# Kernel optimization log

Hardware: AMD Instinct MI355X
Metric: run time of the kernel (lower is better)

## Reference

```python
import jax, jax.numpy as jnp
import numpy as np

D_MODEL = 64
N_HEAD = 4
HEAD_DIM = D_MODEL // N_HEAD  # 16


def setup_inputs() -> dict:
    key = jax.random.key(0)
    ks = jax.random.split(key, 8)
    B, T_dec, T_enc = 16, 1024, 1024
    s = 1.0 / np.sqrt(D_MODEL)
    return {
        "x": jax.random.normal(ks[0], (B, T_dec, D_MODEL), dtype=jnp.float32),
        "encoder_outputs": jax.random.normal(ks[1], (B, T_enc, D_MODEL), dtype=jnp.float32),
        "encoder_outputs_mask": jnp.ones((B, T_enc), dtype=jnp.int32),
        "Wkv": jax.random.normal(ks[2], (D_MODEL, 2 * D_MODEL), dtype=jnp.float32) * s,
        "bkv": jnp.zeros((2 * D_MODEL,), dtype=jnp.float32),
        "Wq": jax.random.normal(ks[3], (D_MODEL, D_MODEL), dtype=jnp.float32) * s,
        "bq": jnp.zeros((D_MODEL,), dtype=jnp.float32),
        "Wproj": jax.random.normal(ks[4], (D_MODEL, D_MODEL), dtype=jnp.float32) * s,
        "bproj": jnp.zeros((D_MODEL,), dtype=jnp.float32),
    }


def reference(x, encoder_outputs, encoder_outputs_mask, Wkv, bkv, Wq, bq, Wproj, bproj):
    B, T_dec, C = x.shape
    T_enc = encoder_outputs.shape[1]
    kv = encoder_outputs @ Wkv + bkv                      # [B, T_enc, 2C]
    k, v = kv[..., :D_MODEL], kv[..., D_MODEL:]          # [B, T_enc, C]
    q = x @ Wq + bq                                      # [B, T_dec, C]
    q = q.reshape(B, T_dec, N_HEAD, HEAD_DIM)
    k = k.reshape(B, T_enc, N_HEAD, HEAD_DIM)
    v = v.reshape(B, T_enc, N_HEAD, HEAD_DIM)
    scale = 1.0 / jnp.sqrt(jnp.asarray(HEAD_DIM, dtype=q.dtype))
    att = jnp.einsum("bqhd,bkhd->bhqk", q, k) * scale    # [B, H, T_dec, T_enc]
    mask = (encoder_outputs_mask == 0)[:, None, None, :]  # [B, 1, 1, T_enc]
    att = jnp.where(mask, jnp.asarray(-jnp.inf, dtype=att.dtype), att)
    att = jax.nn.softmax(att, axis=-1)
    ctx = jnp.einsum("bhqk,bkhd->bqhd", att, v).reshape(B, T_dec, C)
    # dropout is identity at eval time
    return ctx @ Wproj + bproj
```

## Files before the change

kernel.cpp:

```cpp
#include <hip/hip_runtime.h>
#include <hip/hip_bf16.h>
#include <math.h>

#define DM 64
#define NH 4
#define HD 16
#define BATCH 16
#define TSEQ 1024

typedef short bf16x8 __attribute__((ext_vector_type(8)));
typedef float f32x4  __attribute__((ext_vector_type(4)));
typedef float f32x16 __attribute__((ext_vector_type(16)));

__device__ inline short f2bf(float x) {
    __hip_bfloat16 h = __float2bfloat16(x);
    return __builtin_bit_cast(short, h);
}
__device__ inline float bf2f(short s) {
    __hip_bfloat16 h = __builtin_bit_cast(__hip_bfloat16, s);
    return __bfloat162float(h);
}

__global__ __launch_bounds__(256) void proj_kernel(
    const float* __restrict__ x, const float* __restrict__ enc,
    const float* __restrict__ Wkv, const float* __restrict__ bkv,
    const float* __restrict__ Wq,  const float* __restrict__ bq,
    short* __restrict__ qhi, short* __restrict__ qlo,
    short* __restrict__ khi, short* __restrict__ klo,
    short* __restrict__ vt)
{
    const int t = threadIdx.x;
    const int r = blockIdx.x * 256 + t;
    const int b = r >> 10;
    const int trow = r & 1023;
    const int part = blockIdx.y;

    const float* in; const float* W; const float* bias;
    int cb, ldw;
    if (part < 4)      { in = x;   W = Wq;  ldw = 64;  cb = part*16;          bias = bq;  }
    else if (part < 8) { in = enc; W = Wkv; ldw = 128; cb = (part-4)*16;      bias = bkv; }
    else               { in = enc; W = Wkv; ldw = 128; cb = 64 + (part-8)*16; bias = bkv; }

    __shared__ float wsl[64][17];
    for (int idx = t; idx < 1024; idx += 256)
        wsl[idx >> 4][idx & 15] = W[(idx >> 4)*ldw + cb + (idx & 15)];
    __syncthreads();

    float xr[64];
    const float4* inrow = (const float4*)(in + (size_t)r * 64);
    #pragma unroll
    for (int i = 0; i < 16; ++i) {
        float4 v = inrow[i];
        xr[4*i+0]=v.x; xr[4*i+1]=v.y; xr[4*i+2]=v.z; xr[4*i+3]=v.w;
    }

    float acc[16];
    #pragma unroll
    for (int j = 0; j < 16; ++j) acc[j] = bias[cb + j];
    #pragma unroll
    for (int i = 0; i < 64; ++i) {
        float xi = xr[i];
        #pragma unroll
        for (int j = 0; j < 16; ++j) acc[j] += xi * wsl[i][j];
    }

    if (part < 8) {
        const float scale = (part < 4) ? 0.36067376022224085f : 1.0f;
        bf16x8 h0, h1, l0, l1;
        #pragma unroll
        for (int j = 0; j < 16; ++j) {
            float v = acc[j] * scale;
            short hb = f2bf(v);
            short lb = f2bf(v - bf2f(hb));
            if (j < 8) { h0[j] = hb; l0[j] = lb; }
            else       { h1[j-8] = hb; l1[j-8] = lb; }
        }
        const int h = cb >> 4;
        short* dh; short* dl;
        if (part < 4) { dh = qhi; dl = qlo; } else { dh = khi; dl = klo; }
        size_t off = (((size_t)(b*NH + h))*TSEQ + trow)*HD;
        *(bf16x8*)(dh + off)     = h0;
        *(bf16x8*)(dh + off + 8) = h1;
        *(bf16x8*)(dl + off)     = l0;
        *(bf16x8*)(dl + off + 8) = l1;
    } else {
        const int h = part - 8;
        short* base = vt + ((size_t)(b*NH + h)) * HD * TSEQ;
        #pragma unroll
        for (int j = 0; j < 16; ++j)
            base[(size_t)j * TSEQ + trow] = f2bf(acc[j]);
    }
}

__global__ __launch_bounds__(512) void attn_kernel(
    const short* __restrict__ qhi, const short* __restrict__ qlo,
    const short* __restrict__ khi, const short* __restrict__ klo,
    const short* __restrict__ vt,  const int* __restrict__ mask,
    const float* __restrict__ Wproj, const float* __restrict__ bproj,
    float* __restrict__ out)
{
    const int tid  = threadIdx.x;
    const int lane = tid & 63;
    const int wid  = __builtin_amdgcn_readfirstlane(tid >> 6);
    const int h  = wid & 3;
    const int ks = wid >> 2;
    const int qt = blockIdx.x;
    const int b  = blockIdx.y;
    const int qbase = qt * 32;

    __shared__ float Pbuf[8][32][36];
    __shared__ float Cbuf[2][32][68];
    __shared__ float Lbuf[2][NH][32];

    const int l31  = lane & 31;
    const int l15  = lane & 15;
    const int half = lane >> 5;
    const int quad = lane >> 4;

    const size_t qoff = (((size_t)(b*NH + h))*TSEQ + qbase + l31)*HD + half*8;
    const bf16x8 qAh = *(const bf16x8*)(qhi + qoff);
    const bf16x8 qAl = *(const bf16x8*)(qlo + qoff);

    const short* khb = khi + (((size_t)(b*NH + h))*TSEQ + ks*512)*HD;
    const short* klb = klo + (((size_t)(b*NH + h))*TSEQ + ks*512)*HD;
    const short* vtb = vt  + ((size_t)(b*NH + h))*HD*TSEQ + ks*512;
    const int*  mrow = mask + b*TSEQ + ks*512;

    f32x4 ctx0, ctx1;
    #pragma unroll
    for (int i = 0; i < 4; ++i) { ctx0[i] = 0.f; ctx1[i] = 0.f; }
    float lacc[16];
    #pragma unroll
    for (int i = 0; i < 16; ++i) lacc[i] = 0.f;

    float* pmine = &Pbuf[wid][0][0];

    for (int step = 0; step < 16; ++step) {
        const int koff = step * 32;
        const bf16x8 kBh = *(const bf16x8*)(khb + (size_t)(koff + l31)*HD + half*8);
        const bf16x8 kBl = *(const bf16x8*)(klb + (size_t)(koff + l31)*HD + half*8);

        f32x16 S;
        #pragma unroll
        for (int i = 0; i < 16; ++i) S[i] = 0.f;
        S = __builtin_amdgcn_mfma_f32_32x32x16_bf16(qAh, kBh, S, 0, 0, 0);
        S = __builtin_amdgcn_mfma_f32_32x32x16_bf16(qAh, kBl, S, 0, 0, 0);
        S = __builtin_amdgcn_mfma_f32_32x32x16_bf16(qAl, kBh, S, 0, 0, 0);

        const int mk = mrow[koff + l31];
        #pragma unroll
        for (int i = 0; i < 16; ++i) {
            float p = __builtin_amdgcn_exp2f(S[i]);
            p = (mk != 0) ? p : 0.0f;
            lacc[i] += p;
            const int row = (i & 3) + 8*(i >> 2) + 4*half;
            pmine[row*36 + l31] = p;
        }

        const float* pr0 = &Pbuf[wid][l15][quad*8];
        const float* pr1 = &Pbuf[wid][16 + l15][quad*8];
        bf16x8 pA0, pA1;
        #pragma unroll
        for (int j = 0; j < 8; ++j) { pA0[j] = f2bf(pr0[j]); pA1[j] = f2bf(pr1[j]); }

        const bf16x8 vB = *(const bf16x8*)(vtb + (size_t)l15*TSEQ + koff + quad*8);

        ctx0 = __builtin_amdgcn_mfma_f32_16x16x32_bf16(pA0, vB, ctx0, 0, 0, 0);
        ctx1 = __builtin_amdgcn_mfma_f32_16x16x32_bf16(pA1, vB, ctx1, 0, 0, 0);
    }

    #pragma unroll
    for (int off = 1; off < 32; off <<= 1) {
        #pragma unroll
        for (int i = 0; i < 16; ++i)
            lacc[i] += __shfl_xor(lacc[i], off, 64);
    }
    if (l31 == 0) {
        #pragma unroll
        for (int i = 0; i < 16; ++i) {
            const int row = (i & 3) + 8*(i >> 2) + 4*half;
            Lbuf[ks][h][row] = lacc[i];
        }
    }

    #pragma unroll
    for (int rr = 0; rr < 4; ++rr) {
        Cbuf[ks][quad*4 + rr][h*HD + l15]      = ctx0[rr];
        Cbuf[ks][16 + quad*4 + rr][h*HD + l15] = ctx1[rr];
    }
    __syncthreads();

    const int q  = tid >> 4;
    const int cbo = (tid & 15) * 4;
    float linv[NH];
    #pragma unroll
    for (int hh = 0; hh < NH; ++hh)
        linv[hh] = 1.0f / (Lbuf[0][hh][q] + Lbuf[1][hh][q]);

    float o0 = bproj[cbo], o1 = bproj[cbo+1], o2 = bproj[cbo+2], o3 = bproj[cbo+3];
    #pragma unroll
    for (int i = 0; i < 64; ++i) {
        float cv = (Cbuf[0][q][i] + Cbuf[1][q][i]) * linv[i >> 4];
        const float* wr = Wproj + i*DM + cbo;
        o0 += cv*wr[0]; o1 += cv*wr[1]; o2 += cv*wr[2]; o3 += cv*wr[3];
    }
    float4 st; st.x = o0; st.y = o1; st.z = o2; st.w = o3;
    *(float4*)(out + ((size_t)b*TSEQ + qbase + q)*DM + cbo) = st;
}

extern "C" void kernel_launch(void* const* d_in, const int* in_sizes, int n_in,
                              void* d_out, int out_size, void* d_ws, size_t ws_size,
                              hipStream_t stream) {
    const float* x     = (const float*)d_in[0];
    const float* enc   = (const float*)d_in[1];
    const int*   mask  = (const int*)  d_in[2];
    const float* Wkv   = (const float*)d_in[3];
    const float* bkv   = (const float*)d_in[4];
    const float* Wq    = (const float*)d_in[5];
    const float* bq    = (const float*)d_in[6];
    const float* Wproj = (const float*)d_in[7];
    const float* bproj = (const float*)d_in[8];
    float* out = (float*)d_out;

    const size_t SZ = (size_t)BATCH*NH*TSEQ*HD;
    short* qhi = (short*)d_ws;
    short* qlo = qhi + SZ;
    short* khi = qlo + SZ;
    short* klo = khi + SZ;
    short* vt  = klo + SZ;

    proj_kernel<<<dim3(64, 12), dim3(256), 0, stream>>>(
        x, enc, Wkv, bkv, Wq, bq, qhi, qlo, khi, klo, vt);
    attn_kernel<<<dim3(32, 16), dim3(512), 0, stream>>>(
        qhi, qlo, khi, klo, vt, mask, Wproj, bproj, out);
}
```

Measured before the change: 119.9 us.

## Fold softmax row-sum into PV MFMA via ones column and prefetch K/V

The attention kernel now computes P·V with a 32x32x16 MFMA over a padded V^T. The projection kernel writes a row of ones at index 16 of V^T, so the softmax denominator comes out of the same MFMA and the per-lane accumulation and shuffle reduction go away. P is stored as bf16 in shared memory rather than fp32, and the next step's K, V and mask loads are issued before the current step's compute. The projection kernel is retiled to 8 output columns and 2 rows per thread with chunked input prefetch. In exchange, the V^T workspace doubles in size, its padding rows 17-31 are never initialised, and half of the PV MFMA output is wasted.

```diff
diff --git a/kernel.cpp b/kernel.cpp
--- a/kernel.cpp
+++ b/kernel.cpp
@@ -7,16 +7,18 @@
 #define HD 16
 #define BATCH 16
 #define TSEQ 1024
+#define VROWS 32
 
 typedef short bf16x8 __attribute__((ext_vector_type(8)));
+typedef short bf16x4 __attribute__((ext_vector_type(4)));
 typedef float f32x4  __attribute__((ext_vector_type(4)));
 typedef float f32x16 __attribute__((ext_vector_type(16)));
 
-__device__ inline short f2bf(float x) {
+static __device__ inline short f2bf(float x) {
     __hip_bfloat16 h = __float2bfloat16(x);
     return __builtin_bit_cast(short, h);
 }
-__device__ inline float bf2f(short s) {
+static __device__ inline float bf2f(short s) {
     __hip_bfloat16 h = __builtin_bit_cast(__hip_bfloat16, s);
     return __bfloat162float(h);
 }
@@ -30,65 +32,95 @@
     short* __restrict__ vt)
 {
     const int t = threadIdx.x;
-    const int r = blockIdx.x * 256 + t;
-    const int b = r >> 10;
-    const int trow = r & 1023;
     const int part = blockIdx.y;
-
-    const float* in; const float* W; const float* bias;
-    int cb, ldw;
-    if (part < 4)      { in = x;   W = Wq;  ldw = 64;  cb = part*16;          bias = bq;  }
-    else if (part < 8) { in = enc; W = Wkv; ldw = 128; cb = (part-4)*16;      bias = bkv; }
-    else               { in = enc; W = Wkv; ldw = 128; cb = 64 + (part-8)*16; bias = bkv; }
-
-    __shared__ float wsl[64][17];
-    for (int idx = t; idx < 1024; idx += 256)
-        wsl[idx >> 4][idx & 15] = W[(idx >> 4)*ldw + cb + (idx & 15)];
+    const int r0 = blockIdx.x * 512 + t;
+
+    const float* in; const float* W; const float* bias; int cb, ldw;
+    if (part < 8)       { in = x;   W = Wq;  ldw = 64;  cb = part*8;           bias = bq;  }
+    else if (part < 16) { in = enc; W = Wkv; ldw = 128; cb = (part-8)*8;       bias = bkv; }
+    else                { in = enc; W = Wkv; ldw = 128; cb = 64 + (part-16)*8; bias = bkv; }
+
+    const float4* row0 = (const float4*)(in + (size_t)r0*64);
+    const float4* row1 = (const float4*)(in + (size_t)(r0+256)*64);
+
+    float4 xc[2][4];
+    #pragma unroll
+    for (int v4 = 0; v4 < 4; ++v4) { xc[0][v4] = row0[v4]; xc[1][v4] = row1[v4]; }
+
+    __shared__ float wsl[64][8];
+    wsl[t >> 3][t & 7] = W[(t >> 3)*ldw + cb + (t & 7)];
+    {
+        int i1 = t + 256;
+        wsl[i1 >> 3][i1 & 7] = W[(i1 >> 3)*ldw + cb + (i1 & 7)];
+    }
     __syncthreads();
 
-    float xr[64];
-    const float4* inrow = (const float4*)(in + (size_t)r * 64);
-    #pragma unroll
-    for (int i = 0; i < 16; ++i) {
-        float4 v = inrow[i];
-        xr[4*i+0]=v.x; xr[4*i+1]=v.y; xr[4*i+2]=v.z; xr[4*i+3]=v.w;
-    }
-
-    float acc[16];
-    #pragma unroll
-    for (int j = 0; j < 16; ++j) acc[j] = bias[cb + j];
-    #pragma unroll
-    for (int i = 0; i < 64; ++i) {
-        float xi = xr[i];
-        #pragma unroll
-        for (int j = 0; j < 16; ++j) acc[j] += xi * wsl[i][j];
-    }
-
-    if (part < 8) {
-        const float scale = (part < 4) ? 0.36067376022224085f : 1.0f;
-        bf16x8 h0, h1, l0, l1;
-        #pragma unroll
-        for (int j = 0; j < 16; ++j) {
-            float v = acc[j] * scale;
-            short hb = f2bf(v);
-            short lb = f2bf(v - bf2f(hb));
-            if (j < 8) { h0[j] = hb; l0[j] = lb; }
-            else       { h1[j-8] = hb; l1[j-8] = lb; }
-        }
-        const int h = cb >> 4;
-        short* dh; short* dl;
-        if (part < 4) { dh = qhi; dl = qlo; } else { dh = khi; dl = klo; }
-        size_t off = (((size_t)(b*NH + h))*TSEQ + trow)*HD;
-        *(bf16x8*)(dh + off)     = h0;
-        *(bf16x8*)(dh + off + 8) = h1;
-        *(bf16x8*)(dl + off)     = l0;
-        *(bf16x8*)(dl + off + 8) = l1;
+    float acc[2][8];
+    #pragma unroll
+    for (int j = 0; j < 8; ++j) { float bj = bias[cb + j]; acc[0][j] = bj; acc[1][j] = bj; }
+
+    for (int kc = 0; kc < 4; ++kc) {
+        float4 xn[2][4];
+        if (kc < 3) {
+            #pragma unroll
+            for (int v4 = 0; v4 < 4; ++v4) {
+                xn[0][v4] = row0[(kc+1)*4 + v4];
+                xn[1][v4] = row1[(kc+1)*4 + v4];
+            }
+        }
+        #pragma unroll
+        for (int i = 0; i < 16; ++i) {
+            const int k = kc*16 + i;
+            const float4 w0 = ((const float4*)&wsl[k][0])[0];
+            const float4 w1 = ((const float4*)&wsl[k][0])[1];
+            const float xv0 = ((const float*)&xc[0][i >> 2])[i & 3];
+            const float xv1 = ((const float*)&xc[1][i >> 2])[i & 3];
+            acc[0][0] += xv0*w0.x; acc[0][1] += xv0*w0.y; acc[0][2] += xv0*w0.z; acc[0][3] += xv0*w0.w;
+            acc[0][4] += xv0*w1.x; acc[0][5] += xv0*w1.y; acc[0][6] += xv0*w1.z; acc[0][7] += xv0*w1.w;
+            acc[1][0] += xv1*w0.x; acc[1][1] += xv1*w0.y; acc[1][2] += xv1*w0.z; acc[1][3] += xv1*w0.w;
+            acc[1][4] += xv1*w1.x; acc[1][5] += xv1*w1.y; acc[1][6] += xv1*w1.z; acc[1][7] += xv1*w1.w;
+        }
+        if (kc < 3) {
+            #pragma unroll
+            for (int v4 = 0; v4 < 4; ++v4) { xc[0][v4] = xn[0][v4]; xc[1][v4] = xn[1][v4]; }
+        }
+    }
+
+    if (part < 16) {
+        const float scale = (part < 8) ? 0.36067376022224085f : 1.0f;
+        short* dh = (part < 8) ? qhi : khi;
+        short* dl = (part < 8) ? qlo : klo;
+        const int h  = cb >> 4;
+        const int d0 = cb & 15;
+        #pragma unroll
+        for (int rr = 0; rr < 2; ++rr) {
+            const int r = r0 + rr*256;
+            const int b = r >> 10, trow = r & 1023;
+            bf16x8 hv, lv;
+            #pragma unroll
+            for (int j = 0; j < 8; ++j) {
+                float vf = acc[rr][j] * scale;
+                short hb = f2bf(vf);
+                hv[j] = hb;
+                lv[j] = f2bf(vf - bf2f(hb));
+            }
+            size_t off = (((size_t)(b*NH + h))*TSEQ + trow)*HD + d0;
+            *(bf16x8*)(dh + off) = hv;
+            *(bf16x8*)(dl + off) = lv;
+        }
     } else {
-        const int h = part - 8;
-        short* base = vt + ((size_t)(b*NH + h)) * HD * TSEQ;
-        #pragma unroll
-        for (int j = 0; j < 16; ++j)
-            base[(size_t)j * TSEQ + trow] = f2bf(acc[j]);
+        const int h  = (part - 16) >> 1;
+        const int d0 = ((part - 16) & 1) * 8;
+        #pragma unroll
+        for (int rr = 0; rr < 2; ++rr) {
+            const int r = r0 + rr*256;
+            const int b = r >> 10, trow = r & 1023;
+            short* base = vt + ((size_t)(b*NH + h))*VROWS*TSEQ;
+            #pragma unroll
+            for (int j = 0; j < 8; ++j)
+                base[(size_t)(d0 + j)*TSEQ + trow] = f2bf(acc[rr][j]);
+            if (d0 == 8) base[(size_t)16*TSEQ + trow] = (short)0x3F80;
+        }
     }
 }
 
@@ -104,41 +136,43 @@
     const int wid  = __builtin_amdgcn_readfirstlane(tid >> 6);
     const int h  = wid & 3;
     const int ks = wid >> 2;
-    const int qt = blockIdx.x;
+    const int qbase = blockIdx.x * 32;
     const int b  = blockIdx.y;
-    const int qbase = qt * 32;
-
-    __shared__ float Pbuf[8][32][36];
+    const int l31 = lane & 31, half = lane >> 5;
+
+    __shared__ short Pb[8][32][36];
     __shared__ float Cbuf[2][32][68];
     __shared__ float Lbuf[2][NH][32];
-
-    const int l31  = lane & 31;
-    const int l15  = lane & 15;
-    const int half = lane >> 5;
-    const int quad = lane >> 4;
 
     const size_t qoff = (((size_t)(b*NH + h))*TSEQ + qbase + l31)*HD + half*8;
     const bf16x8 qAh = *(const bf16x8*)(qhi + qoff);
     const bf16x8 qAl = *(const bf16x8*)(qlo + qoff);
 
-    const short* khb = khi + (((size_t)(b*NH + h))*TSEQ + ks*512)*HD;
-    const short* klb = klo + (((size_t)(b*NH + h))*TSEQ + ks*512)*HD;
-    const short* vtb = vt  + ((size_t)(b*NH + h))*HD*TSEQ + ks*512;
-    const int*  mrow = mask + b*TSEQ + ks*512;
-
-    f32x4 ctx0, ctx1;
-    #pragma unroll
-    for (int i = 0; i < 4; ++i) { ctx0[i] = 0.f; ctx1[i] = 0.f; }
-    float lacc[16];
-    #pragma unroll
-    for (int i = 0; i < 16; ++i) lacc[i] = 0.f;
-
-    float* pmine = &Pbuf[wid][0][0];
+    const short* khb  = khi + (((size_t)(b*NH + h))*TSEQ + ks*512)*HD;
+    const short* klb  = klo + (((size_t)(b*NH + h))*TSEQ + ks*512)*HD;
+    const short* vtb  = vt  + ((size_t)(b*NH + h))*VROWS*TSEQ + ks*512;
+    const int*   mrow = mask + b*TSEQ + ks*512;
+
+    f32x16 Cacc;
+    #pragma unroll
+    for (int i = 0; i < 16; ++i) Cacc[i] = 0.f;
+
+    short* prow_w = &Pb[wid][0][0];
+    const short* prA = &Pb[wid][l31][0];
+
+    bf16x8 kBh = *(const bf16x8*)(khb + (size_t)l31*HD + half*8);
+    bf16x8 kBl = *(const bf16x8*)(klb + (size_t)l31*HD + half*8);
+    bf16x8 vB0 = *(const bf16x8*)(vtb + (size_t)l31*TSEQ + half*8);
+    bf16x8 vB1 = *(const bf16x8*)(vtb + (size_t)l31*TSEQ + 16 + half*8);
+    int mk = mrow[l31];
 
     for (int step = 0; step < 16; ++step) {
-        const int koff = step * 32;
-        const bf16x8 kBh = *(const bf16x8*)(khb + (size_t)(koff + l31)*HD + half*8);
-        const bf16x8 kBl = *(const bf16x8*)(klb + (size_t)(koff + l31)*HD + half*8);
+        const int nko = ((step < 15) ? step + 1 : 15) * 32;
+        const bf16x8 nkBh = *(const bf16x8*)(khb + (size_t)(nko + l31)*HD + half*8);
+        const bf16x8 nkBl = *(const bf16x8*)(klb + (size_t)(nko + l31)*HD + half*8);
+        const bf16x8 nvB0 = *(const bf16x8*)(vtb + (size_t)l31*TSEQ + nko + half*8);
+        const bf16x8 nvB1 = *(const bf16x8*)(vtb + (size_t)l31*TSEQ + nko + 16 + half*8);
+        const int    nmk  = mrow[nko + l31];
 
         f32x16 S;
         #pragma unroll
@@ -147,50 +181,36 @@
         S = __builtin_amdgcn_mfma_f32_32x32x16_bf16(qAh, kBl, S, 0, 0, 0);
         S = __builtin_amdgcn_mfma_f32_32x32x16_bf16(qAl, kBh, S, 0, 0, 0);
 
-        const int mk = mrow[koff + l31];
         #pragma unroll
         for (int i = 0; i < 16; ++i) {
             float p = __builtin_amdgcn_exp2f(S[i]);
             p = (mk != 0) ? p : 0.0f;
-            lacc[i] += p;
             const int row = (i & 3) + 8*(i >> 2) + 4*half;
-            pmine[row*36 + l31] = p;
-        }
-
-        const float* pr0 = &Pbuf[wid][l15][quad*8];
-        const float* pr1 = &Pbuf[wid][16 + l15][quad*8];
-        bf16x8 pA0, pA1;
-        #pragma unroll
-        for (int j = 0; j < 8; ++j) { pA0[j] = f2bf(pr0[j]); pA1[j] = f2bf(pr1[j]); }
-
-        const bf16x8 vB = *(const bf16x8*)(vtb + (size_t)l15*TSEQ + koff + quad*8);
-
-        ctx0 = __builtin_amdgcn_mfma_f32_16x16x32_bf16(pA0, vB, ctx0, 0, 0, 0);
-        ctx1 = __builtin_amdgcn_mfma_f32_16x16x32_bf16(pA1, vB, ctx1, 0, 0, 0);
-    }
-
-    #pragma unroll
-    for (int off = 1; off < 32; off <<= 1) {
-        #pragma unroll
-        for (int i = 0; i < 16; ++i)
-            lacc[i] += __shfl_xor(lacc[i], off, 64);
-    }
-    if (l31 == 0) {
-        #pragma unroll
-        for (int i = 0; i < 16; ++i) {
-            const int row = (i & 3) + 8*(i >> 2) + 4*half;
-            Lbuf[ks][h][row] = lacc[i];
-        }
-    }
-
-    #pragma unroll
-    for (int rr = 0; rr < 4; ++rr) {
-        Cbuf[ks][quad*4 + rr][h*HD + l15]      = ctx0[rr];
-        Cbuf[ks][16 + quad*4 + rr][h*HD + l15] = ctx1[rr];
+            prow_w[row*36 + l31] = f2bf(p);
+        }
+
+        const bf16x4 a0 = *(const bf16x4*)(prA + half*8);
+        const bf16x4 a1 = *(const bf16x4*)(prA + half*8 + 4);
+        const bf16x4 a2 = *(const bf16x4*)(prA + 16 + half*8);
+        const bf16x4 a3 = *(const bf16x4*)(prA + 16 + half*8 + 4);
+        const bf16x8 pA0 = __builtin_shufflevector(a0, a1, 0, 1, 2, 3, 4, 5, 6, 7);
+        const bf16x8 pA1 = __builtin_shufflevector(a2, a3, 0, 1, 2, 3, 4, 5, 6, 7);
+
+        Cacc = __builtin_amdgcn_mfma_f32_32x32x16_bf16(pA0, vB0, Cacc, 0, 0, 0);
+        Cacc = __builtin_amdgcn_mfma_f32_32x32x16_bf16(pA1, vB1, Cacc, 0, 0, 0);
+
+        kBh = nkBh; kBl = nkBl; vB0 = nvB0; vB1 = nvB1; mk = nmk;
+    }
+
+    #pragma unroll
+    for (int r = 0; r < 16; ++r) {
+        const int row = (r & 3) + 8*(r >> 2) + 4*half;
+        if (l31 < 16)        Cbuf[ks][row][h*HD + l31] = Cacc[r];
+        else if (l31 == 16)  Lbuf[ks][h][row] = Cacc[r];
     }
     __syncthreads();
 
-    const int q  = tid >> 4;
+    const int q   = tid >> 4;
     const int cbo = (tid & 15) * 4;
     float linv[NH];
     #pragma unroll
@@ -201,8 +221,8 @@
     #pragma unroll
     for (int i = 0; i < 64; ++i) {
         float cv = (Cbuf[0][q][i] + Cbuf[1][q][i]) * linv[i >> 4];
-        const float* wr = Wproj + i*DM + cbo;
-        o0 += cv*wr[0]; o1 += cv*wr[1]; o2 += cv*wr[2]; o3 += cv*wr[3];
+        const float4 wr = *(const float4*)(Wproj + i*DM + cbo);
+        o0 += cv*wr.x; o1 += cv*wr.y; o2 += cv*wr.z; o3 += cv*wr.w;
     }
     float4 st; st.x = o0; st.y = o1; st.z = o2; st.w = o3;
     *(float4*)(out + ((size_t)b*TSEQ + qbase + q)*DM + cbo) = st;
@@ -229,7 +249,7 @@
     short* klo = khi + SZ;
     short* vt  = klo + SZ;
 
-    proj_kernel<<<dim3(64, 12), dim3(256), 0, stream>>>(
+    proj_kernel<<<dim3(32, 24), dim3(256), 0, stream>>>(
         x, enc, Wkv, bkv, Wq, bq, qhi, qlo, khi, klo, vt);
     attn_kernel<<<dim3(32, 16), dim3(512), 0, stream>>>(
         qhi, qlo, khi, klo, vt, mask, Wproj, bproj, out);
```

After: 123.2 us. 1.03x slower.

## Fold mask and softmax row-sum into tiled V and use a 32x32 PV MFMA

Applied to the files above, without the earlier changes.

The projection kernel now multiplies V by the key mask and writes it into 32x32 bf16 tiles, with an extra all-ones row (zero where masked). The row sums of the softmax then come out of the PV MFMA as an extra output column. This removes the per-step mask loads, the scalar row-sum accumulation and the cross-lane shuffle reduction. P is stored to LDS as bf16 rather than fp32, and the two 16x16 PV MFMAs become two 32x32x16 MFMAs; the weight reads are also vectorised. In exchange, rows 17-31 of each V tile are left unwritten, which only affects discarded output columns, and the row-sum is now built from bf16-rounded probabilities.

```diff
diff --git a/kernel.cpp b/kernel.cpp
--- a/kernel.cpp
+++ b/kernel.cpp
@@ -9,14 +9,15 @@
 #define TSEQ 1024
 
 typedef short bf16x8 __attribute__((ext_vector_type(8)));
+typedef short bf16x4 __attribute__((ext_vector_type(4)));
 typedef float f32x4  __attribute__((ext_vector_type(4)));
 typedef float f32x16 __attribute__((ext_vector_type(16)));
 
-__device__ inline short f2bf(float x) {
+static __device__ inline short f2bf(float x) {
     __hip_bfloat16 h = __float2bfloat16(x);
     return __builtin_bit_cast(short, h);
 }
-__device__ inline float bf2f(short s) {
+static __device__ inline float bf2f(short s) {
     __hip_bfloat16 h = __builtin_bit_cast(__hip_bfloat16, s);
     return __bfloat162float(h);
 }
@@ -25,59 +26,61 @@
     const float* __restrict__ x, const float* __restrict__ enc,
     const float* __restrict__ Wkv, const float* __restrict__ bkv,
     const float* __restrict__ Wq,  const float* __restrict__ bq,
+    const int* __restrict__ mask,
     short* __restrict__ qhi, short* __restrict__ qlo,
     short* __restrict__ khi, short* __restrict__ klo,
-    short* __restrict__ vt)
+    short* __restrict__ vtt)
 {
     const int t = threadIdx.x;
+    const int part = blockIdx.y;
     const int r = blockIdx.x * 256 + t;
-    const int b = r >> 10;
-    const int trow = r & 1023;
-    const int part = blockIdx.y;
-
-    const float* in; const float* W; const float* bias;
-    int cb, ldw;
+    const int b = r >> 10, trow = r & 1023;
+
+    const float* in; const float* W; const float* bias; int cb, ldw;
     if (part < 4)      { in = x;   W = Wq;  ldw = 64;  cb = part*16;          bias = bq;  }
     else if (part < 8) { in = enc; W = Wkv; ldw = 128; cb = (part-4)*16;      bias = bkv; }
     else               { in = enc; W = Wkv; ldw = 128; cb = 64 + (part-8)*16; bias = bkv; }
 
-    __shared__ float wsl[64][17];
+    __shared__ float wsl[64][16];
     for (int idx = t; idx < 1024; idx += 256)
         wsl[idx >> 4][idx & 15] = W[(idx >> 4)*ldw + cb + (idx & 15)];
+
+    float4 xr[16];
+    const float4* inrow = (const float4*)(in + (size_t)r * 64);
+    #pragma unroll
+    for (int i = 0; i < 16; ++i) xr[i] = inrow[i];
     __syncthreads();
 
-    float xr[64];
-    const float4* inrow = (const float4*)(in + (size_t)r * 64);
-    #pragma unroll
-    for (int i = 0; i < 16; ++i) {
-        float4 v = inrow[i];
-        xr[4*i+0]=v.x; xr[4*i+1]=v.y; xr[4*i+2]=v.z; xr[4*i+3]=v.w;
-    }
-
     float acc[16];
     #pragma unroll
     for (int j = 0; j < 16; ++j) acc[j] = bias[cb + j];
     #pragma unroll
-    for (int i = 0; i < 64; ++i) {
-        float xi = xr[i];
-        #pragma unroll
-        for (int j = 0; j < 16; ++j) acc[j] += xi * wsl[i][j];
+    for (int k = 0; k < 64; ++k) {
+        const float xv = ((const float*)xr)[k];
+        const float4 w0 = ((const float4*)&wsl[k][0])[0];
+        const float4 w1 = ((const float4*)&wsl[k][0])[1];
+        const float4 w2 = ((const float4*)&wsl[k][0])[2];
+        const float4 w3 = ((const float4*)&wsl[k][0])[3];
+        acc[0]  += xv*w0.x; acc[1]  += xv*w0.y; acc[2]  += xv*w0.z; acc[3]  += xv*w0.w;
+        acc[4]  += xv*w1.x; acc[5]  += xv*w1.y; acc[6]  += xv*w1.z; acc[7]  += xv*w1.w;
+        acc[8]  += xv*w2.x; acc[9]  += xv*w2.y; acc[10] += xv*w2.z; acc[11] += xv*w2.w;
+        acc[12] += xv*w3.x; acc[13] += xv*w3.y; acc[14] += xv*w3.z; acc[15] += xv*w3.w;
     }
 
     if (part < 8) {
         const float scale = (part < 4) ? 0.36067376022224085f : 1.0f;
+        short* dh = (part < 4) ? qhi : khi;
+        short* dl = (part < 4) ? qlo : klo;
+        const int h = (part < 4) ? part : (part - 4);
         bf16x8 h0, h1, l0, l1;
         #pragma unroll
         for (int j = 0; j < 16; ++j) {
-            float v = acc[j] * scale;
-            short hb = f2bf(v);
-            short lb = f2bf(v - bf2f(hb));
+            float vf = acc[j] * scale;
+            short hb = f2bf(vf);
+            short lb = f2bf(vf - bf2f(hb));
             if (j < 8) { h0[j] = hb; l0[j] = lb; }
             else       { h1[j-8] = hb; l1[j-8] = lb; }
         }
-        const int h = cb >> 4;
-        short* dh; short* dl;
-        if (part < 4) { dh = qhi; dl = qlo; } else { dh = khi; dl = klo; }
         size_t off = (((size_t)(b*NH + h))*TSEQ + trow)*HD;
         *(bf16x8*)(dh + off)     = h0;
         *(bf16x8*)(dh + off + 8) = h1;
@@ -85,17 +88,20 @@
         *(bf16x8*)(dl + off + 8) = l1;
     } else {
         const int h = part - 8;
-        short* base = vt + ((size_t)(b*NH + h)) * HD * TSEQ;
+        const float mb = (mask[b*TSEQ + trow] != 0) ? 1.0f : 0.0f;
+        short* tile = vtt + ((size_t)(b*NH + h))*32768 + (size_t)(trow >> 5)*1024;
+        const int kw = trow & 31;
         #pragma unroll
         for (int j = 0; j < 16; ++j)
-            base[(size_t)j * TSEQ + trow] = f2bf(acc[j]);
+            tile[j*32 + kw] = f2bf(acc[j] * mb);
+        tile[16*32 + kw] = (mb != 0.0f) ? (short)0x3F80 : (short)0;
     }
 }
 
 __global__ __launch_bounds__(512) void attn_kernel(
     const short* __restrict__ qhi, const short* __restrict__ qlo,
     const short* __restrict__ khi, const short* __restrict__ klo,
-    const short* __restrict__ vt,  const int* __restrict__ mask,
+    const short* __restrict__ vtt,
     const float* __restrict__ Wproj, const float* __restrict__ bproj,
     float* __restrict__ out)
 {
@@ -104,18 +110,13 @@
     const int wid  = __builtin_amdgcn_readfirstlane(tid >> 6);
     const int h  = wid & 3;
     const int ks = wid >> 2;
-    const int qt = blockIdx.x;
+    const int qbase = blockIdx.x * 32;
     const int b  = blockIdx.y;
-    const int qbase = qt * 32;
-
-    __shared__ float Pbuf[8][32][36];
-    __shared__ float Cbuf[2][32][68];
+    const int l31 = lane & 31, half = lane >> 5;
+
+    __shared__ short Pb[8][32][36];
+    __shared__ float Cbuf[2][32][67];
     __shared__ float Lbuf[2][NH][32];
-
-    const int l31  = lane & 31;
-    const int l15  = lane & 15;
-    const int half = lane >> 5;
-    const int quad = lane >> 4;
 
     const size_t qoff = (((size_t)(b*NH + h))*TSEQ + qbase + l31)*HD + half*8;
     const bf16x8 qAh = *(const bf16x8*)(qhi + qoff);
@@ -123,22 +124,22 @@
 
     const short* khb = khi + (((size_t)(b*NH + h))*TSEQ + ks*512)*HD;
     const short* klb = klo + (((size_t)(b*NH + h))*TSEQ + ks*512)*HD;
-    const short* vtb = vt  + ((size_t)(b*NH + h))*HD*TSEQ + ks*512;
-    const int*  mrow = mask + b*TSEQ + ks*512;
-
-    f32x4 ctx0, ctx1;
-    #pragma unroll
-    for (int i = 0; i < 4; ++i) { ctx0[i] = 0.f; ctx1[i] = 0.f; }
-    float lacc[16];
-    #pragma unroll
-    for (int i = 0; i < 16; ++i) lacc[i] = 0.f;
-
-    float* pmine = &Pbuf[wid][0][0];
+    const short* vtb = vtt + ((size_t)(b*NH + h))*32768 + (size_t)ks*16384;
+
+    f32x16 Cacc;
+    #pragma unroll
+    for (int i = 0; i < 16; ++i) Cacc[i] = 0.f;
+
+    short* pw = &Pb[wid][0][0];
+    const short* pr = &Pb[wid][l31][0];
 
     for (int step = 0; step < 16; ++step) {
-        const int koff = step * 32;
-        const bf16x8 kBh = *(const bf16x8*)(khb + (size_t)(koff + l31)*HD + half*8);
-        const bf16x8 kBl = *(const bf16x8*)(klb + (size_t)(koff + l31)*HD + half*8);
+        const int ko = step * 32;
+        const bf16x8 kBh = *(const bf16x8*)(khb + (size_t)(ko + l31)*HD + half*8);
+        const bf16x8 kBl = *(const bf16x8*)(klb + (size_t)(ko + l31)*HD + half*8);
+        const short* tile = vtb + (size_t)step * 1024;
+        const bf16x8 vB0 = *(const bf16x8*)(tile + l31*32 + half*8);
+        const bf16x8 vB1 = *(const bf16x8*)(tile + l31*32 + 16 + half*8);
 
         f32x16 S;
         #pragma unroll
@@ -147,50 +148,33 @@
         S = __builtin_amdgcn_mfma_f32_32x32x16_bf16(qAh, kBl, S, 0, 0, 0);
         S = __builtin_amdgcn_mfma_f32_32x32x16_bf16(qAl, kBh, S, 0, 0, 0);
 
-        const int mk = mrow[koff + l31];
         #pragma unroll
         for (int i = 0; i < 16; ++i) {
-            float p = __builtin_amdgcn_exp2f(S[i]);
-            p = (mk != 0) ? p : 0.0f;
-            lacc[i] += p;
+            const float p = __builtin_amdgcn_exp2f(S[i]);
             const int row = (i & 3) + 8*(i >> 2) + 4*half;
-            pmine[row*36 + l31] = p;
+            pw[row*36 + l31] = f2bf(p);
         }
 
-        const float* pr0 = &Pbuf[wid][l15][quad*8];
-        const float* pr1 = &Pbuf[wid][16 + l15][quad*8];
-        bf16x8 pA0, pA1;
-        #pragma unroll
-        for (int j = 0; j < 8; ++j) { pA0[j] = f2bf(pr0[j]); pA1[j] = f2bf(pr1[j]); }
-
-        const bf16x8 vB = *(const bf16x8*)(vtb + (size_t)l15*TSEQ + koff + quad*8);
-
-        ctx0 = __builtin_amdgcn_mfma_f32_16x16x32_bf16(pA0, vB, ctx0, 0, 0, 0);
-        ctx1 = __builtin_amdgcn_mfma_f32_16x16x32_bf16(pA1, vB, ctx1, 0, 0, 0);
-    }
-
-    #pragma unroll
-    for (int off = 1; off < 32; off <<= 1) {
-        #pragma unroll
-        for (int i = 0; i < 16; ++i)
-            lacc[i] += __shfl_xor(lacc[i], off, 64);
-    }
-    if (l31 == 0) {
-        #pragma unroll
-        for (int i = 0; i < 16; ++i) {
-            const int row = (i & 3) + 8*(i >> 2) + 4*half;
-            Lbuf[ks][h][row] = lacc[i];
-        }
-    }
-
-    #pragma unroll
-    for (int rr = 0; rr < 4; ++rr) {
-        Cbuf[ks][quad*4 + rr][h*HD + l15]      = ctx0[rr];
-        Cbuf[ks][16 + quad*4 + rr][h*HD + l15] = ctx1[rr];
+        const bf16x4 a0 = *(const bf16x4*)(pr + half*8);
+        const bf16x4 a1 = *(const bf16x4*)(pr + half*8 + 4);
+        const bf16x4 a2 = *(const bf16x4*)(pr + 16 + half*8);
+        const bf16x4 a3 = *(const bf16x4*)(pr + 16 + half*8 + 4);
+        const bf16x8 pA0 = __builtin_shufflevector(a0, a1, 0, 1, 2, 3, 4, 5, 6, 7);
+        const bf16x8 pA1 = __builtin_shufflevector(a2, a3, 0, 1, 2, 3, 4, 5, 6, 7);
+
+        Cacc = __builtin_amdgcn_mfma_f32_32x32x16_bf16(pA0, vB0, Cacc, 0, 0, 0);
+        Cacc = __builtin_amdgcn_mfma_f32_32x32x16_bf16(pA1, vB1, Cacc, 0, 0, 0);
+    }
+
+    #pragma unroll
+    for (int r = 0; r < 16; ++r) {
+        const int row = (r & 3) + 8*(r >> 2) + 4*half;
+        if (l31 < 16)        Cbuf[ks][row][h*HD + l31] = Cacc[r];
+        else if (l31 == 16)  Lbuf[ks][h][row] = Cacc[r];
     }
     __syncthreads();
 
-    const int q  = tid >> 4;
+    const int q   = tid >> 4;
     const int cbo = (tid & 15) * 4;
     float linv[NH];
     #pragma unroll
@@ -200,9 +184,9 @@
     float o0 = bproj[cbo], o1 = bproj[cbo+1], o2 = bproj[cbo+2], o3 = bproj[cbo+3];
     #pragma unroll
     for (int i = 0; i < 64; ++i) {
-        float cv = (Cbuf[0][q][i] + Cbuf[1][q][i]) * linv[i >> 4];
-        const float* wr = Wproj + i*DM + cbo;
-        o0 += cv*wr[0]; o1 += cv*wr[1]; o2 += cv*wr[2]; o3 += cv*wr[3];
+        const float cv = (Cbuf[0][q][i] + Cbuf[1][q][i]) * linv[i >> 4];
+        const float4 wr = *(const float4*)(Wproj + i*DM + cbo);
+        o0 += cv*wr.x; o1 += cv*wr.y; o2 += cv*wr.z; o3 += cv*wr.w;
     }
     float4 st; st.x = o0; st.y = o1; st.z = o2; st.w = o3;
     *(float4*)(out + ((size_t)b*TSEQ + qbase + q)*DM + cbo) = st;
@@ -227,10 +211,10 @@
     short* qlo = qhi + SZ;
     short* khi = qlo + SZ;
     short* klo = khi + SZ;
-    short* vt  = klo + SZ;
+    short* vtt = klo + SZ;
 
     proj_kernel<<<dim3(64, 12), dim3(256), 0, stream>>>(
-        x, enc, Wkv, bkv, Wq, bq, qhi, qlo, khi, klo, vt);
+        x, enc, Wkv, bkv, Wq, bq, mask, qhi, qlo, khi, klo, vtt);
     attn_kernel<<<dim3(32, 16), dim3(512), 0, stream>>>(
-        qhi, qlo, khi, klo, vt, mask, Wproj, bproj, out);
-}
+        qhi, qlo, khi, klo, vtt, Wproj, bproj, out);
+}
```

Result: faster. 112.9 us (-5.9%).
